# Kernel optimization log

Measured on AMD Instinct MI355X. Metric: run time of the kernel, lower is better.

The kernel has to match this reference:

```python
import jax, jax.numpy as jnp
import numpy as np

B, L, H, NH, T, WIN = 4, 4096, 256, 8, 64, 16
D = H // NH
NEG_SLOPE = 5.0
MASK_FILL = -1e12


def _leaky(x):
    return jnp.where(x >= 0, x, NEG_SLOPE * x)


def _window_indices():
    # static numpy index construction, mirrors EdgeBlock.self_attn
    off_u = np.concatenate([np.zeros(WIN + 1, np.int64), np.arange(1, WIN + 1)])
    off_d = np.concatenate([np.arange(-WIN, 0), np.zeros(WIN + 1, np.int64)])
    idx_u = np.arange(L)[:, None] + off_u  # [L, 2W+1]
    idx_d = np.arange(L)[:, None] + off_d  # [L, 2W+1]
    idx_mask = (idx_d >= 0) & (idx_u < L)
    return idx_u % L, idx_d % L, idx_mask


def setup_inputs() -> dict:
    key = jax.random.key(0)
    ks = jax.random.split(key, 12)
    s = 1.0 / np.sqrt(H)
    lengths = jnp.array([L, L - 128, L - 512, L - 1024])
    context_mask = jnp.arange(L)[None, :] < lengths[:, None]  # [B, L] bool
    return {
        'context': jax.random.normal(ks[0], (B, L, H), jnp.float32),
        'types': jax.random.normal(ks[1], (B, T, H), jnp.float32),
        'context_mask': context_mask,
        'W_types': jax.random.normal(ks[2], (H, H), jnp.float32) * s,
        'b_types': jnp.zeros((H,), jnp.float32),
        'W_context': jax.random.normal(ks[3], (H, H), jnp.float32) * s,
        'b_context': jnp.zeros((H,), jnp.float32),
        'upon': jax.random.normal(ks[4], (NH, D), jnp.float32) * s,
        'down': jax.random.normal(ks[5], (NH, D), jnp.float32) * s,
        'cross': jax.random.normal(ks[6], (NH, D, D), jnp.float32) * s,
        'W_out': jax.random.normal(ks[7], (H, H), jnp.float32) * s,
        'b_out': jnp.zeros((H,), jnp.float32),
    }


def reference(context, types, context_mask, W_types, b_types, W_context, b_context,
              upon, down, cross, W_out, b_out):
    idx_u, idx_d, idx_mask = _window_indices()

    # head-split projections
    types_h = (types @ W_types + b_types).reshape(B, T, NH, D)      # [B,T,n,d]
    context_h = (context @ W_context + b_context).reshape(B, L, NH, D)  # [B,L,n,d]

    # ---- cross attention scores: context queries over types (EdgeBlock.cross_attn)
    upon_q = jnp.einsum('blnd,nd->bnl', context_h, upon)
    down_t = jnp.einsum('btnd,nd->bnt', types_h, down)
    concat_ct = upon_q[..., None] + down_t[:, :, None, :]           # [B,n,L,T]
    prod_ct = jnp.einsum('blnd,ndh,btnh->bnlt', context_h, cross, types_h)
    types_s = _leaky(concat_ct + prod_ct)                            # [B,n,L,T]

    # ---- windowed self attention scores (EdgeBlock.self_attn)
    down_s = jnp.einsum('blnd,nd->bnl', context_h, down)
    concat_self = upon_q[:, :, idx_u] + down_s[:, :, idx_d]          # [B,n,L,2W+1]
    win_idx = idx_u  # source: cat([indices_d[:, :0], indices_u[:, 0:]]) == indices_u
    wmask = context_mask[:, win_idx] & idx_mask                      # [B,L,2W+1]
    value_h = context_h[:, win_idx]                                  # [B,L,2W+1,n,d]
    prod_self = jnp.einsum('blnd,ndh,blvnh->bnlv', context_h, cross, value_h)
    context_s = jnp.where(wmask[:, None], _leaky(concat_self + prod_self), MASK_FILL)

    # ---- joint softmax over types + window, then aggregate
    weights = jax.nn.softmax(jnp.concatenate([types_s, context_s], axis=-1), axis=-1)
    types_w, context_w = weights[..., :T], weights[..., T:]
    upd_t = jnp.einsum('bnlt,btnd->blnd', types_w, types_h)
    upd_c = jnp.einsum('bnlv,blvnd->blnd', context_w, value_h)
    update = (upd_t + upd_c).reshape(B, L, H)

    # residual + output transform (no_gate=True path: Linear + Tanh)
    return jnp.tanh((update + context) @ W_out + b_out)
```

## Files before the change

### kernel.cpp

```cpp
#include <hip/hip_runtime.h>
#include <cstdint>

#define Bq 4
#define Lq 4096
#define Hq 256
#define NHq 8
#define Tq 64
#define WINq 16
#define Dq 32
#define NSLOTS 33
#define NEG_SLOPE 5.0f
#define MASK_FILL -1e12f
#define TLq 64
#define MB 16

typedef __attribute__((ext_vector_type(8))) short short8;
typedef __attribute__((ext_vector_type(4))) float f32x4;

__device__ __forceinline__ float leaky(float x) { return x >= 0.f ? x : NEG_SLOPE * x; }

__device__ __forceinline__ uint16_t f2bf(float x) {
    uint32_t u = __float_as_uint(x);
    uint32_t r = (u + 0x7fffu + ((u >> 16) & 1u)) >> 16;
    return (uint16_t)r;
}
__device__ __forceinline__ float bf2f(uint16_t h) {
    return __uint_as_float(((uint32_t)h) << 16);
}

__global__ void k_prep(const float* __restrict__ Wc, const float* __restrict__ Wo,
                       uint16_t* __restrict__ pc_hi, uint16_t* __restrict__ pc_lo,
                       uint16_t* __restrict__ po_hi, uint16_t* __restrict__ po_lo,
                       const float* __restrict__ types, const float* __restrict__ Wt,
                       const float* __restrict__ bt, const float* __restrict__ down,
                       float* __restrict__ types_h, float* __restrict__ types_hT,
                       float* __restrict__ down_t) {
    __shared__ float sin[Hq];
    __shared__ float outr[Hq];
    if (blockIdx.x < 128) {
        int wsel = blockIdx.x >> 6;
        int blk = blockIdx.x & 63;
        const float* W = wsel ? Wo : Wc;
        uint16_t* ph = wsel ? po_hi : pc_hi;
        uint16_t* pl = wsel ? po_lo : pc_lo;
        int base = blk * 1024;
        for (int idx = base + threadIdx.x; idx < base + 1024; idx += 256) {
            int j = idx & 7, l = (idx >> 3) & 63, fragi = idx >> 9;
            int kc = fragi & 7, nt = fragi >> 3;
            int k = kc * 32 + (l >> 4) * 8 + j;
            int c = nt * 16 + (l & 15);
            float x = W[k * Hq + c];
            uint16_t h = f2bf(x);
            ph[idx] = h;
            pl[idx] = f2bf(x - bf2f(h));
        }
        return;
    }
    int row = blockIdx.x - 128;
    int h = threadIdx.x;
    int b = row >> 6, t = row & 63;
    sin[h] = types[(size_t)row * Hq + h];
    __syncthreads();
    float acc = bt[h];
    for (int k = 0; k < Hq; k += 4) {
        float4 iv = *(const float4*)&sin[k];
        acc = fmaf(iv.x, Wt[(k + 0) * Hq + h], acc);
        acc = fmaf(iv.y, Wt[(k + 1) * Hq + h], acc);
        acc = fmaf(iv.z, Wt[(k + 2) * Hq + h], acc);
        acc = fmaf(iv.w, Wt[(k + 3) * Hq + h], acc);
    }
    types_h[(size_t)row * Hq + h] = acc;
    types_hT[(size_t)(b * Hq + h) * Tq + t] = acc;
    outr[h] = acc;
    __syncthreads();
    if (h < NHq) {
        float s = 0.f;
        for (int d = 0; d < Dq; ++d) s += outr[h * Dq + d] * down[h * Dq + d];
        down_t[(b * NHq + h) * Tq + t] = s;
    }
}

#define APAD 264
#define OPAD 258
__global__ void __launch_bounds__(256) k_ctx(
        const float* __restrict__ ctx,
        const uint16_t* __restrict__ wp_hi, const uint16_t* __restrict__ wp_lo,
        const float* __restrict__ bc, const float* __restrict__ upon,
        const float* __restrict__ down,
        float* __restrict__ ctx_hT, float* __restrict__ uq,
        float* __restrict__ dsv) {
    int row0 = blockIdx.x * MB;
    int b = row0 >> 12, l0 = row0 & (Lq - 1);
    int tid = threadIdx.x;
    int w = tid >> 6, l = tid & 63;
    __shared__ __align__(16) char smem_raw[MB * APAD * 4];
    uint16_t* a_hi = (uint16_t*)smem_raw;
    uint16_t* a_lo = a_hi + MB * APAD;
    float* outb = (float*)smem_raw;

    {
        const float4* src = (const float4*)(ctx + (size_t)row0 * Hq);
#pragma unroll
        for (int j = 0; j < 4; ++j) {
            int f = tid + j * 256;
            int r = f >> 6, cg = f & 63;
            float4 v = src[f];
            uint16_t h0 = f2bf(v.x), h1 = f2bf(v.y), h2 = f2bf(v.z), h3 = f2bf(v.w);
            ushort4 hh = {h0, h1, h2, h3};
            ushort4 ll = {f2bf(v.x - bf2f(h0)), f2bf(v.y - bf2f(h1)),
                          f2bf(v.z - bf2f(h2)), f2bf(v.w - bf2f(h3))};
            *(ushort4*)&a_hi[r * APAD + cg * 4] = hh;
            *(ushort4*)&a_lo[r * APAD + cg * 4] = ll;
        }
    }
    __syncthreads();

    int nt0 = w * 4;
    int m = l & 15, quad = l >> 4;
    f32x4 acc[4];
#pragma unroll
    for (int t = 0; t < 4; ++t) acc[t] = (f32x4){0.f, 0.f, 0.f, 0.f};
#pragma unroll
    for (int kc = 0; kc < 8; ++kc) {
        short8 ah = *(const short8*)&a_hi[m * APAD + kc * 32 + quad * 8];
        short8 al = *(const short8*)&a_lo[m * APAD + kc * 32 + quad * 8];
#pragma unroll
        for (int t = 0; t < 4; ++t) {
            int fragi = (nt0 + t) * 8 + kc;
            short8 wh = *(const short8*)&wp_hi[fragi * 512 + l * 8];
            short8 wl = *(const short8*)&wp_lo[fragi * 512 + l * 8];
            acc[t] = __builtin_amdgcn_mfma_f32_16x16x32_bf16(ah, wh, acc[t], 0, 0, 0);
            acc[t] = __builtin_amdgcn_mfma_f32_16x16x32_bf16(ah, wl, acc[t], 0, 0, 0);
            acc[t] = __builtin_amdgcn_mfma_f32_16x16x32_bf16(al, wh, acc[t], 0, 0, 0);
        }
    }
    __syncthreads();

#pragma unroll
    for (int t = 0; t < 4; ++t) {
        int col = (nt0 + t) * 16 + m;
        float bv = bc[col];
#pragma unroll
        for (int r = 0; r < 4; ++r)
            outb[(quad * 4 + r) * OPAD + col] = acc[t][r] + bv;
    }
    __syncthreads();

    if (tid < MB * NHq) {
        int r = tid >> 3, n = tid & 7;
        float su = 0.f, sd = 0.f;
        for (int d = 0; d < Dq; ++d) {
            float v = outb[r * OPAD + n * Dq + d];
            su += v * upon[n * Dq + d];
            sd += v * down[n * Dq + d];
        }
        uq[(b * NHq + n) * Lq + l0 + r] = su;
        dsv[(b * NHq + n) * Lq + l0 + r] = sd;
    }
    {
        float* dst = ctx_hT + (size_t)(b * Hq + tid) * Lq + l0;
#pragma unroll
        for (int j = 0; j < MB / 4; ++j) {
            float4 o;
            o.x = outb[(4 * j + 0) * OPAD + tid];
            o.y = outb[(4 * j + 1) * OPAD + tid];
            o.z = outb[(4 * j + 2) * OPAD + tid];
            o.w = outb[(4 * j + 3) * OPAD + tid];
            ((float4*)dst)[j] = o;
        }
    }
}

__global__ void __launch_bounds__(256, 5) k_attn(
        const float* __restrict__ ctx_hT, const float* __restrict__ types_h,
        const float* __restrict__ types_hT, const float* __restrict__ cross,
        const float* __restrict__ uq, const float* __restrict__ dsv,
        const float* __restrict__ dt, const unsigned char* __restrict__ maskp,
        float* __restrict__ update) {
    int blk = blockIdx.x;
    int lt = blk & 63, n = (blk >> 6) & 7, b = blk >> 9;
    int l0 = lt * TLq;
    int tid = threadIdx.x;
    int ls = tid >> 2;
    int q  = tid & 3;
    int pl = l0 + ls;
    bool mask_b8 = (maskp[1] != 0);

    __shared__ float chx_s[32 * 97];
    __shared__ float crs_s[32 * 36];
    __shared__ float dots_s[64 * 19];
    __shared__ float tts2_s[64 * 36 + 16];
    __shared__ float uqe[96], dsve[96], maskf[96], dts[64];

    {
        int d = tid >> 3, k = tid & 7;
        const float* grow = ctx_hT + ((size_t)(b * NHq + n) * Dq + d) * Lq;
        float* lrow = &chx_s[d * 97 + k * 12];
        if (l0 >= 16 && l0 <= Lq - 80) {
            const float4* g = (const float4*)(grow + (l0 - 16) + k * 12);
            float4 v0 = g[0], v1 = g[1], v2 = g[2];
            lrow[0] = v0.x; lrow[1] = v0.y; lrow[2]  = v0.z; lrow[3]  = v0.w;
            lrow[4] = v1.x; lrow[5] = v1.y; lrow[6]  = v1.z; lrow[7]  = v1.w;
            lrow[8] = v2.x; lrow[9] = v2.y; lrow[10] = v2.z; lrow[11] = v2.w;
        } else {
#pragma unroll
            for (int m = 0; m < 12; ++m) {
                int gl = l0 - 16 + k * 12 + m;
                int glw = (gl < 0) ? gl + Lq : ((gl >= Lq) ? gl - Lq : gl);
                lrow[m] = grow[glw];
            }
        }
    }
    {
        float4 v = ((const float4*)(cross + n * (Dq * Dq)))[tid];
        float* p = &crs_s[(tid >> 3) * 36 + (tid & 7) * 4];
        p[0] = v.x; p[1] = v.y; p[2] = v.z; p[3] = v.w;
    }
    {
        int t = tid >> 2, c4 = tid & 3;
        const float4* src = (const float4*)(types_h + (size_t)(b * Tq + t) * Hq
                                            + n * Dq + 8 * c4);
        float* p = &tts2_s[t * 36 + 4 * (t >> 4) + 8 * c4];
        ((float4*)p)[0] = src[0];
        ((float4*)p)[1] = src[1];
    }
    if (tid < 96) {
        int gl = l0 - 16 + tid;
        int glw = (gl < 0) ? gl + Lq : ((gl >= Lq) ? gl - Lq : gl);
        uqe[tid] = uq[(b * NHq + n) * Lq + glw];
        unsigned char mb = mask_b8 ? maskp[b * Lq + glw]
                                   : maskp[(size_t)(b * Lq + glw) * 4];
        maskf[tid] = mb ? 1.f : 0.f;
    } else if (tid < 192) {
        int j = tid - 96;
        int gl = l0 - 16 + j;
        int glw = (gl < 0) ? gl + Lq : ((gl >= Lq) ? gl - Lq : gl);
        dsve[j] = dsv[(b * NHq + n) * Lq + glw];
    } else {
        dts[tid - 192] = dt[(b * NHq + n) * Tq + (tid - 192)];
    }
    __syncthreads();

    float a[8];
#pragma unroll
    for (int ii = 0; ii < 8; ++ii) a[ii] = 0.f;
#pragma unroll 2
    for (int d = 0; d < Dq; ++d) {
        float chv = chx_s[d * 97 + ls + 16];
        const float4* cp = (const float4*)(&crs_s[d * 36 + 8 * q]);
        float4 c0 = cp[0], c1 = cp[1];
        a[0] = fmaf(chv, c0.x, a[0]); a[1] = fmaf(chv, c0.y, a[1]);
        a[2] = fmaf(chv, c0.z, a[2]); a[3] = fmaf(chv, c0.w, a[3]);
        a[4] = fmaf(chv, c1.x, a[4]); a[5] = fmaf(chv, c1.y, a[5]);
        a[6] = fmaf(chv, c1.z, a[6]); a[7] = fmaf(chv, c1.w, a[7]);
    }

    float dot_self;
    {
#pragma unroll
        for (int u = 0; u < 17; ++u) {
            float acc = 0.f;
#pragma unroll
            for (int k = 0; k < 8; ++k)
                acc = fmaf(a[k], chx_s[(8 * q + k) * 97 + ls + 16 + u], acc);
            acc += __shfl_xor(acc, 1);
            acc += __shfl_xor(acc, 2);
            if (u == 0) dot_self = acc;
            else if (q == 0) dots_s[ls * 19 + u] = acc;
        }
    }

    float uq_l = uqe[ls + 16];
    float dsv_l = dsve[ls + 16];
    float cmask = maskf[ls + 16];

    int tb = 16 * q;
    float st[16];
#pragma unroll
    for (int j = 0; j < 16; ++j) st[j] = 0.f;
#pragma unroll
    for (int half = 0; half < 2; ++half) {
        float crf[16];
#pragma unroll
        for (int k = 0; k < 16; ++k)
            crf[k] = __shfl(a[k & 7], 2 * half + (k >> 3), 4);
#pragma unroll 4
        for (int j = 0; j < 16; ++j) {
            const float4* rp =
                (const float4*)&tts2_s[(tb + j) * 36 + 4 * q + 16 * half];
            float4 v0 = rp[0], v1 = rp[1], v2 = rp[2], v3 = rp[3];
            st[j] = fmaf(crf[0],  v0.x, st[j]); st[j] = fmaf(crf[1],  v0.y, st[j]);
            st[j] = fmaf(crf[2],  v0.z, st[j]); st[j] = fmaf(crf[3],  v0.w, st[j]);
            st[j] = fmaf(crf[4],  v1.x, st[j]); st[j] = fmaf(crf[5],  v1.y, st[j]);
            st[j] = fmaf(crf[6],  v1.z, st[j]); st[j] = fmaf(crf[7],  v1.w, st[j]);
            st[j] = fmaf(crf[8],  v2.x, st[j]); st[j] = fmaf(crf[9],  v2.y, st[j]);
            st[j] = fmaf(crf[10], v2.z, st[j]); st[j] = fmaf(crf[11], v2.w, st[j]);
            st[j] = fmaf(crf[12], v3.x, st[j]); st[j] = fmaf(crf[13], v3.y, st[j]);
            st[j] = fmaf(crf[14], v3.z, st[j]); st[j] = fmaf(crf[15], v3.w, st[j]);
        }
    }
#pragma unroll
    for (int j = 0; j < 16; ++j)
        st[j] = leaky(uq_l + dts[tb + j] + st[j]);

    int nv = (q == 0) ? 5 : 4;
    float su[4];
#pragma unroll
    for (int j = 0; j < 4; ++j) {
        int u = q + 1 + 4 * j;
        bool ok = (pl + u < Lq) && (maskf[ls + 16 + u] > 0.5f);
        su[j] = ok ? leaky(uqe[ls + 16 + u] + dsv_l + dots_s[ls * 19 + u])
                   : MASK_FILL;
    }

    float m = st[0];
#pragma unroll
    for (int j = 1; j < 16; ++j) m = fmaxf(m, st[j]);
#pragma unroll
    for (int j = 0; j < 5; ++j) {
        if (j < nv) {
            int v = q + 4 * j;
            if ((pl + v >= 16) && (cmask > 0.5f))
                m = fmaxf(m, leaky(uq_l + dsve[ls + v] + dot_self));
        }
    }
#pragma unroll
    for (int j = 0; j < 4; ++j) m = fmaxf(m, su[j]);
    m = fmaxf(m, __shfl_xor(m, 1));
    m = fmaxf(m, __shfl_xor(m, 2));
    float sum = 0.f, wself = 0.f;
#pragma unroll
    for (int j = 0; j < 16; ++j) { st[j] = __expf(st[j] - m); sum += st[j]; }
#pragma unroll
    for (int j = 0; j < 5; ++j) {
        if (j < nv) {
            int v = q + 4 * j;
            if ((pl + v >= 16) && (cmask > 0.5f)) {
                float e = __expf(leaky(uq_l + dsve[ls + v] + dot_self) - m);
                wself += e; sum += e;
            }
        }
    }
#pragma unroll
    for (int j = 0; j < 4; ++j)  { su[j] = __expf(su[j] - m); sum += su[j]; }
    sum += __shfl_xor(sum, 1);
    sum += __shfl_xor(sum, 2);
    float inv = 1.f / sum;
#pragma unroll
    for (int j = 0; j < 16; ++j) st[j] *= inv;
    wself *= inv;
#pragma unroll
    for (int j = 0; j < 4; ++j)  su[j] *= inv;

    float* dstrow = update + (size_t)(b * Lq + pl) * Hq + n * Dq;
#pragma unroll
    for (int c = 0; c < 4; ++c) {
        float u8[8];
#pragma unroll
        for (int e = 0; e < 8; ++e) u8[e] = 0.f;
#pragma unroll 2
        for (int j = 0; j < 16; ++j) {
            const float* vp = &tts2_s[(tb + j) * 36 + 4 * q + 8 * c];
            float4 a0 = ((const float4*)vp)[0];
            float4 a1 = ((const float4*)vp)[1];
            float wt = st[j];
            u8[0] = fmaf(wt, a0.x, u8[0]); u8[1] = fmaf(wt, a0.y, u8[1]);
            u8[2] = fmaf(wt, a0.z, u8[2]); u8[3] = fmaf(wt, a0.w, u8[3]);
            u8[4] = fmaf(wt, a1.x, u8[4]); u8[5] = fmaf(wt, a1.y, u8[5]);
            u8[6] = fmaf(wt, a1.z, u8[6]); u8[7] = fmaf(wt, a1.w, u8[7]);
        }
#pragma unroll
        for (int e = 0; e < 8; ++e)
            u8[e] = fmaf(wself, chx_s[(8 * c + e) * 97 + ls + 16], u8[e]);
#pragma unroll
        for (int j = 0; j < 4; ++j) {
            float wu = su[j];
            int u = q + 1 + 4 * j;
#pragma unroll
            for (int e = 0; e < 8; ++e)
                u8[e] = fmaf(wu, chx_s[(8 * c + e) * 97 + ls + 16 + u], u8[e]);
        }
#pragma unroll
        for (int e = 0; e < 8; ++e) {
            u8[e] += __shfl_xor(u8[e], 1);
            u8[e] += __shfl_xor(u8[e], 2);
        }
        if (q == c) {
            ((float4*)(dstrow + 8 * c))[0] = make_float4(u8[0], u8[1], u8[2], u8[3]);
            ((float4*)(dstrow + 8 * c))[1] = make_float4(u8[4], u8[5], u8[6], u8[7]);
        }
    }
}

__global__ void __launch_bounds__(256) k_out(
        const float* __restrict__ update, const float* __restrict__ ctx,
        const uint16_t* __restrict__ wp_hi, const uint16_t* __restrict__ wp_lo,
        const float* __restrict__ bo, float* __restrict__ out) {
    int row0 = blockIdx.x * MB;
    int tid = threadIdx.x;
    int w = tid >> 6, l = tid & 63;
    __shared__ __align__(16) char smem_raw[MB * APAD * 4];
    uint16_t* a_hi = (uint16_t*)smem_raw;
    uint16_t* a_lo = a_hi + MB * APAD;

    {
        const float4* s0 = (const float4*)(update + (size_t)row0 * Hq);
        const float4* s1 = (const float4*)(ctx + (size_t)row0 * Hq);
#pragma unroll
        for (int j = 0; j < 4; ++j) {
            int f = tid + j * 256;
            int r = f >> 6, cg = f & 63;
            float4 a = s0[f], bv = s1[f];
            float4 v; v.x = a.x + bv.x; v.y = a.y + bv.y;
            v.z = a.z + bv.z; v.w = a.w + bv.w;
            uint16_t h0 = f2bf(v.x), h1 = f2bf(v.y), h2 = f2bf(v.z), h3 = f2bf(v.w);
            ushort4 hh = {h0, h1, h2, h3};
            ushort4 ll = {f2bf(v.x - bf2f(h0)), f2bf(v.y - bf2f(h1)),
                          f2bf(v.z - bf2f(h2)), f2bf(v.w - bf2f(h3))};
            *(ushort4*)&a_hi[r * APAD + cg * 4] = hh;
            *(ushort4*)&a_lo[r * APAD + cg * 4] = ll;
        }
    }
    __syncthreads();

    int nt0 = w * 4;
    int m = l & 15, quad = l >> 4;
    f32x4 acc[4];
#pragma unroll
    for (int t = 0; t < 4; ++t) acc[t] = (f32x4){0.f, 0.f, 0.f, 0.f};
#pragma unroll
    for (int kc = 0; kc < 8; ++kc) {
        short8 ah = *(const short8*)&a_hi[m * APAD + kc * 32 + quad * 8];
        short8 al = *(const short8*)&a_lo[m * APAD + kc * 32 + quad * 8];
#pragma unroll
        for (int t = 0; t < 4; ++t) {
            int fragi = (nt0 + t) * 8 + kc;
            short8 wh = *(const short8*)&wp_hi[fragi * 512 + l * 8];
            short8 wl = *(const short8*)&wp_lo[fragi * 512 + l * 8];
            acc[t] = __builtin_amdgcn_mfma_f32_16x16x32_bf16(ah, wh, acc[t], 0, 0, 0);
            acc[t] = __builtin_amdgcn_mfma_f32_16x16x32_bf16(ah, wl, acc[t], 0, 0, 0);
            acc[t] = __builtin_amdgcn_mfma_f32_16x16x32_bf16(al, wh, acc[t], 0, 0, 0);
        }
    }
#pragma unroll
    for (int t = 0; t < 4; ++t) {
        int col = (nt0 + t) * 16 + m;
        float bv = bo[col];
#pragma unroll
        for (int r = 0; r < 4; ++r)
            out[(size_t)(row0 + quad * 4 + r) * Hq + col] = tanhf(acc[t][r] + bv);
    }
}

extern "C" void kernel_launch(void* const* d_in, const int* in_sizes, int n_in,
                              void* d_out, int out_size, void* d_ws, size_t ws_size,
                              hipStream_t stream) {
    const float* context   = (const float*)d_in[0];
    const float* types     = (const float*)d_in[1];
    const unsigned char* cmask = (const unsigned char*)d_in[2];
    const float* W_types   = (const float*)d_in[3];
    const float* b_types   = (const float*)d_in[4];
    const float* W_context = (const float*)d_in[5];
    const float* b_context = (const float*)d_in[6];
    const float* upon      = (const float*)d_in[7];
    const float* down      = (const float*)d_in[8];
    const float* cross     = (const float*)d_in[9];
    const float* W_out     = (const float*)d_in[10];
    const float* b_out     = (const float*)d_in[11];
    float* out = (float*)d_out;
    float* ws  = (float*)d_ws;

    float* ctx_hT   = ws;
    float* update   = ws + 4194304;
// ... 22 lines not shown
```

Baseline: 190.0 us.

## Compute attention aggregation with split-bf16 MFMA instead of scalar FMAs

Rewrites the weighted aggregation in k_attn (types weights times types values, window weights times context values) as 16x16x32 bf16 MFMA products. Each operand is split into hi and lo bf16 parts and three products are summed to keep near-fp32 accuracy. The window-score dot products stay in registers instead of a shared buffer. Shared memory is now one aliased buffer, which adds several barriers, and launch bounds drop from 5 to 4 blocks per SM. The added bf16 conversion cost and extra syncs may offset the reduced FMA and LDS traffic.

```diff
diff --git a/kernel.cpp b/kernel.cpp
--- a/kernel.cpp
+++ b/kernel.cpp
@@ -8,7 +8,6 @@
 #define Tq 64
 #define WINq 16
 #define Dq 32
-#define NSLOTS 33
 #define NEG_SLOPE 5.0f
 #define MASK_FILL -1e12f
 #define TLq 64
@@ -171,7 +170,11 @@
     }
 }
 
-__global__ void __launch_bounds__(256, 5) k_attn(
+#define WAT_STRIDE 72
+#define TTVT_STRIDE 72
+#define CHVT_STRIDE 104
+#define WAW_STRIDE 48
+__global__ void __launch_bounds__(256, 4) k_attn(
         const float* __restrict__ ctx_hT, const float* __restrict__ types_h,
         const float* __restrict__ types_hT, const float* __restrict__ cross,
         const float* __restrict__ uq, const float* __restrict__ dsv,
@@ -186,12 +189,24 @@
     int pl = l0 + ls;
     bool mask_b8 = (maskp[1] != 0);
 
-    __shared__ float chx_s[32 * 97];
-    __shared__ float crs_s[32 * 36];
-    __shared__ float dots_s[64 * 19];
-    __shared__ float tts2_s[64 * 36 + 16];
-    __shared__ float uqe[96], dsve[96], maskf[96], dts[64];
-
+    __shared__ __align__(16) char smem[36928];
+    float* chx_s  = (float*)(smem);
+    float* crs_s  = (float*)(smem + 12416);
+    float* tts2_s = (float*)(smem + 17024);
+    uint16_t* waT_hi  = (uint16_t*)(smem);
+    uint16_t* waT_lo  = (uint16_t*)(smem + 9216);
+    uint16_t* chvt_hi = (uint16_t*)(smem);
+    uint16_t* chvt_lo = (uint16_t*)(smem + 6656);
+    uint16_t* waw_hi  = (uint16_t*)(smem + 13312);
+    uint16_t* waw_lo  = (uint16_t*)(smem + 19456);
+    uint16_t* ttvt_hi = (uint16_t*)(smem + 26304);
+    uint16_t* ttvt_lo = (uint16_t*)(smem + 30912);
+    float* uqe   = (float*)(smem + 35520);
+    float* dsve  = (float*)(smem + 35904);
+    float* maskf = (float*)(smem + 36288);
+    float* dts   = (float*)(smem + 36672);
+
+    float chvv[12];
     {
         int d = tid >> 3, k = tid & 7;
         const float* grow = ctx_hT + ((size_t)(b * NHq + n) * Dq + d) * Lq;
@@ -199,17 +214,19 @@
         if (l0 >= 16 && l0 <= Lq - 80) {
             const float4* g = (const float4*)(grow + (l0 - 16) + k * 12);
             float4 v0 = g[0], v1 = g[1], v2 = g[2];
-            lrow[0] = v0.x; lrow[1] = v0.y; lrow[2]  = v0.z; lrow[3]  = v0.w;
-            lrow[4] = v1.x; lrow[5] = v1.y; lrow[6]  = v1.z; lrow[7]  = v1.w;
-            lrow[8] = v2.x; lrow[9] = v2.y; lrow[10] = v2.z; lrow[11] = v2.w;
+            chvv[0] = v0.x; chvv[1] = v0.y; chvv[2]  = v0.z; chvv[3]  = v0.w;
+            chvv[4] = v1.x; chvv[5] = v1.y; chvv[6]  = v1.z; chvv[7]  = v1.w;
+            chvv[8] = v2.x; chvv[9] = v2.y; chvv[10] = v2.z; chvv[11] = v2.w;
         } else {
 #pragma unroll
             for (int m = 0; m < 12; ++m) {
                 int gl = l0 - 16 + k * 12 + m;
                 int glw = (gl < 0) ? gl + Lq : ((gl >= Lq) ? gl - Lq : gl);
-                lrow[m] = grow[glw];
+                chvv[m] = grow[glw];
             }
         }
+#pragma unroll
+        for (int m = 0; m < 12; ++m) lrow[m] = chvv[m];
     }
     {
         float4 v = ((const float4*)(cross + n * (Dq * Dq)))[tid];
@@ -223,6 +240,23 @@
         float* p = &tts2_s[t * 36 + 4 * (t >> 4) + 8 * c4];
         ((float4*)p)[0] = src[0];
         ((float4*)p)[1] = src[1];
+    }
+    {
+        int d = tid >> 3, tc8 = (tid & 7) * 8;
+        const float* src = types_hT + ((size_t)(b * Hq) + n * Dq + d) * Tq + tc8;
+        float4 v0 = *(const float4*)src;
+        float4 v1 = *(const float4*)(src + 4);
+        float vv[8] = {v0.x, v0.y, v0.z, v0.w, v1.x, v1.y, v1.z, v1.w};
+        uint hp[4], lp[4];
+#pragma unroll
+        for (int jj = 0; jj < 4; ++jj) {
+            uint16_t h0 = f2bf(vv[2*jj]), h1 = f2bf(vv[2*jj+1]);
+            uint16_t e0 = f2bf(vv[2*jj] - bf2f(h0)), e1 = f2bf(vv[2*jj+1] - bf2f(h1));
+            hp[jj] = (uint)h0 | ((uint)h1 << 16);
+            lp[jj] = (uint)e0 | ((uint)e1 << 16);
+        }
+        *(uint4*)&ttvt_hi[d * TTVT_STRIDE + tc8] = make_uint4(hp[0], hp[1], hp[2], hp[3]);
+        *(uint4*)&ttvt_lo[d * TTVT_STRIDE + tc8] = make_uint4(lp[0], lp[1], lp[2], lp[3]);
     }
     if (tid < 96) {
         int gl = l0 - 16 + tid;
@@ -255,7 +289,7 @@
         a[6] = fmaf(chv, c1.z, a[6]); a[7] = fmaf(chv, c1.w, a[7]);
     }
 
-    float dot_self;
+    float dot_self, sud[4];
     {
 #pragma unroll
         for (int u = 0; u < 17; ++u) {
@@ -266,7 +300,7 @@
             acc += __shfl_xor(acc, 1);
             acc += __shfl_xor(acc, 2);
             if (u == 0) dot_self = acc;
-            else if (q == 0) dots_s[ls * 19 + u] = acc;
+            else if (((u - 1) & 3) == q) sud[(u - 1) >> 2] = acc;
         }
     }
 
@@ -309,7 +343,7 @@
     for (int j = 0; j < 4; ++j) {
         int u = q + 1 + 4 * j;
         bool ok = (pl + u < Lq) && (maskf[ls + 16 + u] > 0.5f);
-        su[j] = ok ? leaky(uqe[ls + 16 + u] + dsv_l + dots_s[ls * 19 + u])
+        su[j] = ok ? leaky(uqe[ls + 16 + u] + dsv_l + sud[j])
                    : MASK_FILL;
     }
 
@@ -351,44 +385,116 @@
     wself *= inv;
 #pragma unroll
     for (int j = 0; j < 4; ++j)  su[j] *= inv;
-
-    float* dstrow = update + (size_t)(b * Lq + pl) * Hq + n * Dq;
-#pragma unroll
-    for (int c = 0; c < 4; ++c) {
-        float u8[8];
-#pragma unroll
-        for (int e = 0; e < 8; ++e) u8[e] = 0.f;
-#pragma unroll 2
-        for (int j = 0; j < 16; ++j) {
-            const float* vp = &tts2_s[(tb + j) * 36 + 4 * q + 8 * c];
-            float4 a0 = ((const float4*)vp)[0];
-            float4 a1 = ((const float4*)vp)[1];
-            float wt = st[j];
-            u8[0] = fmaf(wt, a0.x, u8[0]); u8[1] = fmaf(wt, a0.y, u8[1]);
-            u8[2] = fmaf(wt, a0.z, u8[2]); u8[3] = fmaf(wt, a0.w, u8[3]);
-            u8[4] = fmaf(wt, a1.x, u8[4]); u8[5] = fmaf(wt, a1.y, u8[5]);
-            u8[6] = fmaf(wt, a1.z, u8[6]); u8[7] = fmaf(wt, a1.w, u8[7]);
-        }
-#pragma unroll
-        for (int e = 0; e < 8; ++e)
-            u8[e] = fmaf(wself, chx_s[(8 * c + e) * 97 + ls + 16], u8[e]);
+    wself += __shfl_xor(wself, 1);
+    wself += __shfl_xor(wself, 2);
+
+    __syncthreads();
+
+    {
+        uint hp[8], lp[8];
+#pragma unroll
+        for (int jj = 0; jj < 8; ++jj) {
+            uint16_t h0 = f2bf(st[2*jj]), h1 = f2bf(st[2*jj+1]);
+            uint16_t e0 = f2bf(st[2*jj] - bf2f(h0)), e1 = f2bf(st[2*jj+1] - bf2f(h1));
+            hp[jj] = (uint)h0 | ((uint)h1 << 16);
+            lp[jj] = (uint)e0 | ((uint)e1 << 16);
+        }
+        uint16_t* hb = &waT_hi[ls * WAT_STRIDE + tb];
+        uint16_t* lb = &waT_lo[ls * WAT_STRIDE + tb];
+        *(uint4*)hb       = make_uint4(hp[0], hp[1], hp[2], hp[3]);
+        *(uint4*)(hb + 8) = make_uint4(hp[4], hp[5], hp[6], hp[7]);
+        *(uint4*)lb       = make_uint4(lp[0], lp[1], lp[2], lp[3]);
+        *(uint4*)(lb + 8) = make_uint4(lp[4], lp[5], lp[6], lp[7]);
+    }
+    __syncthreads();
+
+    int wv = tid >> 6;
+    int lane = tid & 63;
+    int mrow = lane & 15, chunk = lane >> 4;
+    f32x4 acc0 = (f32x4){0.f, 0.f, 0.f, 0.f};
+    f32x4 acc1 = (f32x4){0.f, 0.f, 0.f, 0.f};
+#pragma unroll
+    for (int ks = 0; ks < 2; ++ks) {
+        short8 bh = *(const short8*)&waT_hi[(16*wv + mrow) * WAT_STRIDE + 32*ks + 8*chunk];
+        short8 bl = *(const short8*)&waT_lo[(16*wv + mrow) * WAT_STRIDE + 32*ks + 8*chunk];
+        short8 a0h = *(const short8*)&ttvt_hi[mrow * TTVT_STRIDE + 32*ks + 8*chunk];
+        short8 a0l = *(const short8*)&ttvt_lo[mrow * TTVT_STRIDE + 32*ks + 8*chunk];
+        short8 a1h = *(const short8*)&ttvt_hi[(16 + mrow) * TTVT_STRIDE + 32*ks + 8*chunk];
+        short8 a1l = *(const short8*)&ttvt_lo[(16 + mrow) * TTVT_STRIDE + 32*ks + 8*chunk];
+        acc0 = __builtin_amdgcn_mfma_f32_16x16x32_bf16(a0h, bh, acc0, 0, 0, 0);
+        acc0 = __builtin_amdgcn_mfma_f32_16x16x32_bf16(a0l, bh, acc0, 0, 0, 0);
+        acc0 = __builtin_amdgcn_mfma_f32_16x16x32_bf16(a0h, bl, acc0, 0, 0, 0);
+        acc1 = __builtin_amdgcn_mfma_f32_16x16x32_bf16(a1h, bh, acc1, 0, 0, 0);
+        acc1 = __builtin_amdgcn_mfma_f32_16x16x32_bf16(a1l, bh, acc1, 0, 0, 0);
+        acc1 = __builtin_amdgcn_mfma_f32_16x16x32_bf16(a1h, bl, acc1, 0, 0, 0);
+    }
+    __syncthreads();
+
+    {
+        int d = tid >> 3, k = tid & 7;
+        uint hp[6], lp[6];
+#pragma unroll
+        for (int jj = 0; jj < 6; ++jj) {
+            uint16_t h0 = f2bf(chvv[2*jj]), h1 = f2bf(chvv[2*jj+1]);
+            uint16_t e0 = f2bf(chvv[2*jj] - bf2f(h0)), e1 = f2bf(chvv[2*jj+1] - bf2f(h1));
+            hp[jj] = (uint)h0 | ((uint)h1 << 16);
+            lp[jj] = (uint)e0 | ((uint)e1 << 16);
+        }
+        uint16_t* hb = &chvt_hi[d * CHVT_STRIDE + k * 12];
+        uint16_t* lb = &chvt_lo[d * CHVT_STRIDE + k * 12];
+        *(uint2*)(hb)     = make_uint2(hp[0], hp[1]);
+        *(uint2*)(hb + 4) = make_uint2(hp[2], hp[3]);
+        *(uint2*)(hb + 8) = make_uint2(hp[4], hp[5]);
+        *(uint2*)(lb)     = make_uint2(lp[0], lp[1]);
+        *(uint2*)(lb + 4) = make_uint2(lp[2], lp[3]);
+        *(uint2*)(lb + 8) = make_uint2(lp[4], lp[5]);
+    }
+    {
+        float4 z = make_float4(0.f, 0.f, 0.f, 0.f);
+        float4* wz = (float4*)waw_hi;
+        for (int i = tid; i < 768; i += 256) wz[i] = z;
+    }
+    __syncthreads();
+
+    {
+        int jself = (ls & 15) + 16;
 #pragma unroll
         for (int j = 0; j < 4; ++j) {
-            float wu = su[j];
-            int u = q + 1 + 4 * j;
-#pragma unroll
-            for (int e = 0; e < 8; ++e)
-                u8[e] = fmaf(wu, chx_s[(8 * c + e) * 97 + ls + 16 + u], u8[e]);
-        }
-#pragma unroll
-        for (int e = 0; e < 8; ++e) {
-            u8[e] += __shfl_xor(u8[e], 1);
-            u8[e] += __shfl_xor(u8[e], 2);
-        }
-        if (q == c) {
-            ((float4*)(dstrow + 8 * c))[0] = make_float4(u8[0], u8[1], u8[2], u8[3]);
-            ((float4*)(dstrow + 8 * c))[1] = make_float4(u8[4], u8[5], u8[6], u8[7]);
-        }
+            int col = jself + q + 1 + 4 * j;
+            float v = su[j];
+            uint16_t h = f2bf(v);
+            waw_hi[ls * WAW_STRIDE + col] = h;
+            waw_lo[ls * WAW_STRIDE + col] = f2bf(v - bf2f(h));
+        }
+        if (q == 0) {
+            uint16_t h = f2bf(wself);
+            waw_hi[ls * WAW_STRIDE + jself] = h;
+            waw_lo[ls * WAW_STRIDE + jself] = f2bf(wself - bf2f(h));
+        }
+    }
+    __syncthreads();
+
+    {
+        short8 bh = *(const short8*)&waw_hi[(16*wv + mrow) * WAW_STRIDE + 16 + 8*chunk];
+        short8 bl = *(const short8*)&waw_lo[(16*wv + mrow) * WAW_STRIDE + 16 + 8*chunk];
+        int kabs = 16*wv + 16 + 8*chunk;
+        short8 a0h = *(const short8*)&chvt_hi[mrow * CHVT_STRIDE + kabs];
+        short8 a0l = *(const short8*)&chvt_lo[mrow * CHVT_STRIDE + kabs];
+        short8 a1h = *(const short8*)&chvt_hi[(16 + mrow) * CHVT_STRIDE + kabs];
+        short8 a1l = *(const short8*)&chvt_lo[(16 + mrow) * CHVT_STRIDE + kabs];
+        acc0 = __builtin_amdgcn_mfma_f32_16x16x32_bf16(a0h, bh, acc0, 0, 0, 0);
+        acc0 = __builtin_amdgcn_mfma_f32_16x16x32_bf16(a0l, bh, acc0, 0, 0, 0);
+        acc0 = __builtin_amdgcn_mfma_f32_16x16x32_bf16(a0h, bl, acc0, 0, 0, 0);
+        acc1 = __builtin_amdgcn_mfma_f32_16x16x32_bf16(a1h, bh, acc1, 0, 0, 0);
+        acc1 = __builtin_amdgcn_mfma_f32_16x16x32_bf16(a1l, bh, acc1, 0, 0, 0);
+        acc1 = __builtin_amdgcn_mfma_f32_16x16x32_bf16(a1h, bl, acc1, 0, 0, 0);
+    }
+
+    {
+        int lcol = l0 + 16 * wv + mrow;
+        float* dst = update + (size_t)(b * Lq + lcol) * Hq + n * Dq + 4 * chunk;
+        *(float4*)dst        = make_float4(acc0[0], acc0[1], acc0[2], acc0[3]);
+        *(float4*)(dst + 16) = make_float4(acc1[0], acc1[1], acc1[2], acc1[3]);
     }
 }
 
```

Result: faster. 177.9 us (-6.4%).

## Rewrite attention kernel with split-bf16 MFMA matmuls for scores and aggregation

Applied to the files above, without the earlier changes.

Replaces the scalar FMA attention kernel with MFMA 16x16x32 bf16 instructions. Each fp32 operand is split into hi/lo bf16 pairs and combined with three MFMAs to keep close to fp32 accuracy. The cross projection, type scores, window scores and weighted aggregation all become small matrix products staged through a reused shared-memory buffer. The occupancy hint drops from 5 to 3 blocks per SU because of the larger shared footprint. The split-precision conversion and extra syncs add overhead and a small accuracy risk.

```diff
diff --git a/kernel.cpp b/kernel.cpp
--- a/kernel.cpp
+++ b/kernel.cpp
@@ -8,7 +8,6 @@
 #define Tq 64
 #define WINq 16
 #define Dq 32
-#define NSLOTS 33
 #define NEG_SLOPE 5.0f
 #define MASK_FILL -1e12f
 #define TLq 64
@@ -171,7 +170,7 @@
     }
 }
 
-__global__ void __launch_bounds__(256, 5) k_attn(
+__global__ void __launch_bounds__(256, 3) k_attn(
         const float* __restrict__ ctx_hT, const float* __restrict__ types_h,
         const float* __restrict__ types_hT, const float* __restrict__ cross,
         const float* __restrict__ uq, const float* __restrict__ dsv,
@@ -181,214 +180,327 @@
     int lt = blk & 63, n = (blk >> 6) & 7, b = blk >> 9;
     int l0 = lt * TLq;
     int tid = threadIdx.x;
-    int ls = tid >> 2;
-    int q  = tid & 3;
-    int pl = l0 + ls;
+    int g = tid >> 6;
+    int lane = tid & 63;
+    int Q = lane >> 4, s = lane & 15;
     bool mask_b8 = (maskp[1] != 0);
 
-    __shared__ float chx_s[32 * 97];
-    __shared__ float crs_s[32 * 36];
-    __shared__ float dots_s[64 * 19];
-    __shared__ float tts2_s[64 * 36 + 16];
-    __shared__ float uqe[96], dsve[96], maskf[96], dts[64];
-
-    {
-        int d = tid >> 3, k = tid & 7;
-        const float* grow = ctx_hT + ((size_t)(b * NHq + n) * Dq + d) * Lq;
-        float* lrow = &chx_s[d * 97 + k * 12];
-        if (l0 >= 16 && l0 <= Lq - 80) {
-            const float4* g = (const float4*)(grow + (l0 - 16) + k * 12);
-            float4 v0 = g[0], v1 = g[1], v2 = g[2];
-            lrow[0] = v0.x; lrow[1] = v0.y; lrow[2]  = v0.z; lrow[3]  = v0.w;
-            lrow[4] = v1.x; lrow[5] = v1.y; lrow[6]  = v1.z; lrow[7]  = v1.w;
-            lrow[8] = v2.x; lrow[9] = v2.y; lrow[10] = v2.z; lrow[11] = v2.w;
+    __shared__ __align__(16) char smem[53952];
+    uint16_t* TT_hi     = (uint16_t*)(smem);
+    uint16_t* TT_lo     = (uint16_t*)(smem + 5120);
+    uint16_t* chxT_hi   = (uint16_t*)(smem + 10240);
+    uint16_t* chxT_lo   = (uint16_t*)(smem + 16640);
+    uint16_t* waT_hi    = (uint16_t*)(smem);
+    uint16_t* waT_lo    = (uint16_t*)(smem + 9216);
+    uint16_t* crossT_hi = (uint16_t*)(smem + 23040);
+    uint16_t* crossT_lo = (uint16_t*)(smem + 25600);
+    uint16_t* crle_hi   = (uint16_t*)(smem + 23040);
+    uint16_t* crle_lo   = (uint16_t*)(smem + 28160);
+    uint16_t* waw_hi    = (uint16_t*)(smem + 23040);
+    uint16_t* waw_lo    = (uint16_t*)(smem + 28160);
+    uint16_t* chvt_hi   = (uint16_t*)(smem + 33280);
+    uint16_t* chvt_lo   = (uint16_t*)(smem + 38400);
+    uint16_t* ttvt_hi   = (uint16_t*)(smem + 43520);
+    uint16_t* ttvt_lo   = (uint16_t*)(smem + 48128);
+    float* uqe   = (float*)(smem + 52736);
+    float* dsve  = (float*)(smem + 53056);
+    float* maskf = (float*)(smem + 53376);
+    float* dts   = (float*)(smem + 53696);
+
+    {
+        int d_ = tid >> 3, k_ = tid & 7, base = k_ * 10;
+        const float* grow = ctx_hT + ((size_t)(b * NHq + n) * Dq + d_) * Lq;
+        float cv[10];
+        if (l0 <= Lq - 80) {
+            const float2* g2 = (const float2*)(grow + l0 + base);
+#pragma unroll
+            for (int j = 0; j < 5; ++j) { float2 v = g2[j]; cv[2*j] = v.x; cv[2*j+1] = v.y; }
         } else {
 #pragma unroll
-            for (int m = 0; m < 12; ++m) {
-                int gl = l0 - 16 + k * 12 + m;
-                int glw = (gl < 0) ? gl + Lq : ((gl >= Lq) ? gl - Lq : gl);
-                lrow[m] = grow[glw];
+            for (int m = 0; m < 10; ++m) {
+                int gl = l0 + base + m;
+                cv[m] = grow[gl >= Lq ? gl - Lq : gl];
             }
         }
-    }
-    {
+        uint16_t hh[10], ll[10];
+#pragma unroll
+        for (int m = 0; m < 10; ++m) {
+            hh[m] = f2bf(cv[m]);
+            ll[m] = f2bf(cv[m] - bf2f(hh[m]));
+        }
+#pragma unroll
+        for (int j = 0; j < 5; ++j) {
+            *(uint*)&chvt_hi[d_ * 80 + base + 2*j] = (uint)hh[2*j] | ((uint)hh[2*j+1] << 16);
+            *(uint*)&chvt_lo[d_ * 80 + base + 2*j] = (uint)ll[2*j] | ((uint)ll[2*j+1] << 16);
+        }
+#pragma unroll
+        for (int m = 0; m < 10; ++m) {
+            chxT_hi[(base + m) * 40 + d_] = hh[m];
+            chxT_lo[(base + m) * 40 + d_] = ll[m];
+        }
+    }
+    {
+        int d_ = tid >> 3, e4 = (tid & 7) * 4;
         float4 v = ((const float4*)(cross + n * (Dq * Dq)))[tid];
-        float* p = &crs_s[(tid >> 3) * 36 + (tid & 7) * 4];
-        p[0] = v.x; p[1] = v.y; p[2] = v.z; p[3] = v.w;
-    }
-    {
-        int t = tid >> 2, c4 = tid & 3;
-        const float4* src = (const float4*)(types_h + (size_t)(b * Tq + t) * Hq
-                                            + n * Dq + 8 * c4);
-        float* p = &tts2_s[t * 36 + 4 * (t >> 4) + 8 * c4];
-        ((float4*)p)[0] = src[0];
-        ((float4*)p)[1] = src[1];
-    }
-    if (tid < 96) {
-        int gl = l0 - 16 + tid;
-        int glw = (gl < 0) ? gl + Lq : ((gl >= Lq) ? gl - Lq : gl);
+        float vv[4] = {v.x, v.y, v.z, v.w};
+#pragma unroll
+        for (int j = 0; j < 4; ++j) {
+            uint16_t h = f2bf(vv[j]);
+            crossT_hi[(e4 + j) * 40 + d_] = h;
+            crossT_lo[(e4 + j) * 40 + d_] = f2bf(vv[j] - bf2f(h));
+        }
+    }
+    {
+        int t = tid >> 2, c8 = (tid & 3) * 8;
+        const float* src = types_h + (size_t)(b * Tq + t) * Hq + n * Dq + c8;
+        float4 v0 = *(const float4*)src, v1 = *(const float4*)(src + 4);
+        float vv[8] = {v0.x, v0.y, v0.z, v0.w, v1.x, v1.y, v1.z, v1.w};
+        uint hp[4], lp[4];
+#pragma unroll
+        for (int j = 0; j < 4; ++j) {
+            uint16_t h0 = f2bf(vv[2*j]), h1 = f2bf(vv[2*j+1]);
+            hp[j] = (uint)h0 | ((uint)h1 << 16);
+            lp[j] = (uint)f2bf(vv[2*j] - bf2f(h0)) | ((uint)f2bf(vv[2*j+1] - bf2f(h1)) << 16);
+        }
+        *(uint4*)&TT_hi[t * 40 + c8] = make_uint4(hp[0], hp[1], hp[2], hp[3]);
+        *(uint4*)&TT_lo[t * 40 + c8] = make_uint4(lp[0], lp[1], lp[2], lp[3]);
+    }
+    {
+        int d_ = tid >> 3, t8 = (tid & 7) * 8;
+        const float* src = types_hT + ((size_t)(b * Hq) + n * Dq + d_) * Tq + t8;
+        float4 v0 = *(const float4*)src, v1 = *(const float4*)(src + 4);
+        float vv[8] = {v0.x, v0.y, v0.z, v0.w, v1.x, v1.y, v1.z, v1.w};
+        uint hp[4], lp[4];
+#pragma unroll
+        for (int j = 0; j < 4; ++j) {
+            uint16_t h0 = f2bf(vv[2*j]), h1 = f2bf(vv[2*j+1]);
+            hp[j] = (uint)h0 | ((uint)h1 << 16);
+            lp[j] = (uint)f2bf(vv[2*j] - bf2f(h0)) | ((uint)f2bf(vv[2*j+1] - bf2f(h1)) << 16);
+        }
+        *(uint4*)&ttvt_hi[d_ * 72 + t8] = make_uint4(hp[0], hp[1], hp[2], hp[3]);
+        *(uint4*)&ttvt_lo[d_ * 72 + t8] = make_uint4(lp[0], lp[1], lp[2], lp[3]);
+    }
+    if (tid < 80) {
+        int gl = l0 + tid;
+        int glw = gl >= Lq ? gl - Lq : gl;
         uqe[tid] = uq[(b * NHq + n) * Lq + glw];
         unsigned char mb = mask_b8 ? maskp[b * Lq + glw]
                                    : maskp[(size_t)(b * Lq + glw) * 4];
         maskf[tid] = mb ? 1.f : 0.f;
-    } else if (tid < 192) {
-        int j = tid - 96;
-        int gl = l0 - 16 + j;
-        int glw = (gl < 0) ? gl + Lq : ((gl >= Lq) ? gl - Lq : gl);
-        dsve[j] = dsv[(b * NHq + n) * Lq + glw];
-    } else {
+    } else if (tid >= 96 && tid < 176) {
+        int i = tid - 96;
+        int gl = l0 - 16 + i;
+        int glw = gl < 0 ? gl + Lq : (gl >= Lq ? gl - Lq : gl);
+        dsve[i] = dsv[(b * NHq + n) * Lq + glw];
+    } else if (tid >= 192) {
         dts[tid - 192] = dt[(b * NHq + n) * Tq + (tid - 192)];
     }
     __syncthreads();
 
-    float a[8];
-#pragma unroll
-    for (int ii = 0; ii < 8; ++ii) a[ii] = 0.f;
-#pragma unroll 2
-    for (int d = 0; d < Dq; ++d) {
-        float chv = chx_s[d * 97 + ls + 16];
-        const float4* cp = (const float4*)(&crs_s[d * 36 + 8 * q]);
-        float4 c0 = cp[0], c1 = cp[1];
-        a[0] = fmaf(chv, c0.x, a[0]); a[1] = fmaf(chv, c0.y, a[1]);
-        a[2] = fmaf(chv, c0.z, a[2]); a[3] = fmaf(chv, c0.w, a[3]);
-        a[4] = fmaf(chv, c1.x, a[4]); a[5] = fmaf(chv, c1.y, a[5]);
-        a[6] = fmaf(chv, c1.z, a[6]); a[7] = fmaf(chv, c1.w, a[7]);
-    }
-
-    float dot_self;
-    {
-#pragma unroll
-        for (int u = 0; u < 17; ++u) {
-            float acc = 0.f;
-#pragma unroll
-            for (int k = 0; k < 8; ++k)
-                acc = fmaf(a[k], chx_s[(8 * q + k) * 97 + ls + 16 + u], acc);
-            acc += __shfl_xor(acc, 1);
-            acc += __shfl_xor(acc, 2);
-            if (u == 0) dot_self = acc;
-            else if (q == 0) dots_s[ls * 19 + u] = acc;
-        }
-    }
-
-    float uq_l = uqe[ls + 16];
-    float dsv_l = dsve[ls + 16];
-    float cmask = maskf[ls + 16];
-
-    int tb = 16 * q;
-    float st[16];
-#pragma unroll
-    for (int j = 0; j < 16; ++j) st[j] = 0.f;
-#pragma unroll
-    for (int half = 0; half < 2; ++half) {
-        float crf[16];
-#pragma unroll
-        for (int k = 0; k < 16; ++k)
-            crf[k] = __shfl(a[k & 7], 2 * half + (k >> 3), 4);
-#pragma unroll 4
-        for (int j = 0; j < 16; ++j) {
-            const float4* rp =
-                (const float4*)&tts2_s[(tb + j) * 36 + 4 * q + 16 * half];
-            float4 v0 = rp[0], v1 = rp[1], v2 = rp[2], v3 = rp[3];
-            st[j] = fmaf(crf[0],  v0.x, st[j]); st[j] = fmaf(crf[1],  v0.y, st[j]);
-            st[j] = fmaf(crf[2],  v0.z, st[j]); st[j] = fmaf(crf[3],  v0.w, st[j]);
-            st[j] = fmaf(crf[4],  v1.x, st[j]); st[j] = fmaf(crf[5],  v1.y, st[j]);
-            st[j] = fmaf(crf[6],  v1.z, st[j]); st[j] = fmaf(crf[7],  v1.w, st[j]);
-            st[j] = fmaf(crf[8],  v2.x, st[j]); st[j] = fmaf(crf[9],  v2.y, st[j]);
-            st[j] = fmaf(crf[10], v2.z, st[j]); st[j] = fmaf(crf[11], v2.w, st[j]);
-            st[j] = fmaf(crf[12], v3.x, st[j]); st[j] = fmaf(crf[13], v3.y, st[j]);
-            st[j] = fmaf(crf[14], v3.z, st[j]); st[j] = fmaf(crf[15], v3.w, st[j]);
-        }
-    }
-#pragma unroll
-    for (int j = 0; j < 16; ++j)
-        st[j] = leaky(uq_l + dts[tb + j] + st[j]);
-
-    int nv = (q == 0) ? 5 : 4;
-    float su[4];
-#pragma unroll
-    for (int j = 0; j < 4; ++j) {
-        int u = q + 1 + 4 * j;
-        bool ok = (pl + u < Lq) && (maskf[ls + 16 + u] > 0.5f);
-        su[j] = ok ? leaky(uqe[ls + 16 + u] + dsv_l + dots_s[ls * 19 + u])
-                   : MASK_FILL;
-    }
-
-    float m = st[0];
-#pragma unroll
-    for (int j = 1; j < 16; ++j) m = fmaxf(m, st[j]);
-#pragma unroll
-    for (int j = 0; j < 5; ++j) {
-        if (j < nv) {
-            int v = q + 4 * j;
-            if ((pl + v >= 16) && (cmask > 0.5f))
-                m = fmaxf(m, leaky(uq_l + dsve[ls + v] + dot_self));
-        }
-    }
-#pragma unroll
-    for (int j = 0; j < 4; ++j) m = fmaxf(m, su[j]);
-    m = fmaxf(m, __shfl_xor(m, 1));
-    m = fmaxf(m, __shfl_xor(m, 2));
-    float sum = 0.f, wself = 0.f;
-#pragma unroll
-    for (int j = 0; j < 16; ++j) { st[j] = __expf(st[j] - m); sum += st[j]; }
-#pragma unroll
-    for (int j = 0; j < 5; ++j) {
-        if (j < nv) {
-            int v = q + 4 * j;
-            if ((pl + v >= 16) && (cmask > 0.5f)) {
-                float e = __expf(leaky(uq_l + dsve[ls + v] + dot_self) - m);
-                wself += e; sum += e;
-            }
-        }
-    }
-#pragma unroll
-    for (int j = 0; j < 4; ++j)  { su[j] = __expf(su[j] - m); sum += su[j]; }
-    sum += __shfl_xor(sum, 1);
-    sum += __shfl_xor(sum, 2);
-    float inv = 1.f / sum;
-#pragma unroll
-    for (int j = 0; j < 16; ++j) st[j] *= inv;
-    wself *= inv;
-#pragma unroll
-    for (int j = 0; j < 4; ++j)  su[j] *= inv;
-
-    float* dstrow = update + (size_t)(b * Lq + pl) * Hq + n * Dq;
-#pragma unroll
-    for (int c = 0; c < 4; ++c) {
-        float u8[8];
-#pragma unroll
-        for (int e = 0; e < 8; ++e) u8[e] = 0.f;
-#pragma unroll 2
-        for (int j = 0; j < 16; ++j) {
-            const float* vp = &tts2_s[(tb + j) * 36 + 4 * q + 8 * c];
-            float4 a0 = ((const float4*)vp)[0];
-            float4 a1 = ((const float4*)vp)[1];
-            float wt = st[j];
-            u8[0] = fmaf(wt, a0.x, u8[0]); u8[1] = fmaf(wt, a0.y, u8[1]);
-            u8[2] = fmaf(wt, a0.z, u8[2]); u8[3] = fmaf(wt, a0.w, u8[3]);
-            u8[4] = fmaf(wt, a1.x, u8[4]); u8[5] = fmaf(wt, a1.y, u8[5]);
-            u8[6] = fmaf(wt, a1.z, u8[6]); u8[7] = fmaf(wt, a1.w, u8[7]);
-        }
-#pragma unroll
-        for (int e = 0; e < 8; ++e)
-            u8[e] = fmaf(wself, chx_s[(8 * c + e) * 97 + ls + 16], u8[e]);
-#pragma unroll
-        for (int j = 0; j < 4; ++j) {
-            float wu = su[j];
-            int u = q + 1 + 4 * j;
-#pragma unroll
-            for (int e = 0; e < 8; ++e)
-                u8[e] = fmaf(wu, chx_s[(8 * c + e) * 97 + ls + 16 + u], u8[e]);
-        }
-#pragma unroll
-        for (int e = 0; e < 8; ++e) {
-            u8[e] += __shfl_xor(u8[e], 1);
-            u8[e] += __shfl_xor(u8[e], 2);
-        }
-        if (q == c) {
-            ((float4*)(dstrow + 8 * c))[0] = make_float4(u8[0], u8[1], u8[2], u8[3]);
-            ((float4*)(dstrow + 8 * c))[1] = make_float4(u8[4], u8[5], u8[6], u8[7]);
-        }
+    f32x4 cr0 = (f32x4){0.f, 0.f, 0.f, 0.f};
+    f32x4 cr1 = (f32x4){0.f, 0.f, 0.f, 0.f};
+    {
+        short8 axh = *(const short8*)&chxT_hi[(16*g + s) * 40 + 8*Q];
+        short8 axl = *(const short8*)&chxT_lo[(16*g + s) * 40 + 8*Q];
+        short8 b0h = *(const short8*)&crossT_hi[s * 40 + 8*Q];
+        short8 b0l = *(const short8*)&crossT_lo[s * 40 + 8*Q];
+        short8 b1h = *(const short8*)&crossT_hi[(16 + s) * 40 + 8*Q];
+        short8 b1l = *(const short8*)&crossT_lo[(16 + s) * 40 + 8*Q];
+        cr0 = __builtin_amdgcn_mfma_f32_16x16x32_bf16(axh, b0h, cr0, 0, 0, 0);
+        cr0 = __builtin_amdgcn_mfma_f32_16x16x32_bf16(axl, b0h, cr0, 0, 0, 0);
+        cr0 = __builtin_amdgcn_mfma_f32_16x16x32_bf16(axh, b0l, cr0, 0, 0, 0);
+        cr1 = __builtin_amdgcn_mfma_f32_16x16x32_bf16(axh, b1h, cr1, 0, 0, 0);
+        cr1 = __builtin_amdgcn_mfma_f32_16x16x32_bf16(axl, b1h, cr1, 0, 0, 0);
+        cr1 = __builtin_amdgcn_mfma_f32_16x16x32_bf16(axh, b1l, cr1, 0, 0, 0);
+    }
+    __syncthreads();
+
+#pragma unroll
+    for (int r = 0; r < 4; ++r) {
+        int row = 16*g + 4*Q + r;
+        uint16_t h0 = f2bf(cr0[r]);
+        crle_hi[row * 40 + s] = h0;
+        crle_lo[row * 40 + s] = f2bf(cr0[r] - bf2f(h0));
+        uint16_t h1 = f2bf(cr1[r]);
+        crle_hi[row * 40 + 16 + s] = h1;
+        crle_lo[row * 40 + 16 + s] = f2bf(cr1[r] - bf2f(h1));
+    }
+
+    f32x4 p2[4], p3[2];
+#pragma unroll
+    for (int c = 0; c < 4; ++c) p2[c] = (f32x4){0.f, 0.f, 0.f, 0.f};
+#pragma unroll
+    for (int t_ = 0; t_ < 2; ++t_) p3[t_] = (f32x4){0.f, 0.f, 0.f, 0.f};
+    {
+        short8 cah = *(const short8*)&crle_hi[(16*g + s) * 40 + 8*Q];
+        short8 cal = *(const short8*)&crle_lo[(16*g + s) * 40 + 8*Q];
+#pragma unroll
+        for (int c = 0; c < 4; ++c) {
+            short8 bh = *(const short8*)&TT_hi[(s + 16*c) * 40 + 8*Q];
+            short8 bl = *(const short8*)&TT_lo[(s + 16*c) * 40 + 8*Q];
+            p2[c] = __builtin_amdgcn_mfma_f32_16x16x32_bf16(cah, bh, p2[c], 0, 0, 0);
+            p2[c] = __builtin_amdgcn_mfma_f32_16x16x32_bf16(cal, bh, p2[c], 0, 0, 0);
+            p2[c] = __builtin_amdgcn_mfma_f32_16x16x32_bf16(cah, bl, p2[c], 0, 0, 0);
+        }
+#pragma unroll
+        for (int t_ = 0; t_ < 2; ++t_) {
+            short8 bh = *(const short8*)&chxT_hi[(16*g + 16*t_ + s) * 40 + 8*Q];
+            short8 bl = *(const short8*)&chxT_lo[(16*g + 16*t_ + s) * 40 + 8*Q];
+            p3[t_] = __builtin_amdgcn_mfma_f32_16x16x32_bf16(cah, bh, p3[t_], 0, 0, 0);
+            p3[t_] = __builtin_amdgcn_mfma_f32_16x16x32_bf16(cal, bh, p3[t_], 0, 0, 0);
+            p3[t_] = __builtin_amdgcn_mfma_f32_16x16x32_bf16(cah, bl, p3[t_], 0, 0, 0);
+        }
+    }
+
+    float uqr[4], cmr[4], dsr[4], dd[4];
+    *(float4*)uqr = *(const float4*)&uqe[16*g + 4*Q];
+    *(float4*)cmr = *(const float4*)&maskf[16*g + 4*Q];
+    *(float4*)dsr = *(const float4*)&dsve[16*g + 4*Q + 16];
+#pragma unroll
+    for (int r = 0; r < 4; ++r) dd[r] = dsve[16*g + 4*Q + s + r];
+    float dtv[4], uw[2], mw[2];
+#pragma unroll
+    for (int c = 0; c < 4; ++c) dtv[c] = dts[s + 16*c];
+#pragma unroll
+    for (int t_ = 0; t_ < 2; ++t_) {
+        uw[t_] = uqe[16*g + s + 16*t_];
+        mw[t_] = maskf[16*g + s + 16*t_];
+    }
+    float dsb[4];
+#pragma unroll
+    for (int r = 0; r < 4; ++r) dsb[r] = __shfl(p3[0][r], 20*Q + r);
+
+    float stt[4][4], rup[2][4], rdn[4], rdn16[4];
+#pragma unroll
+    for (int c = 0; c < 4; ++c)
+#pragma unroll
+        for (int r = 0; r < 4; ++r)
+            stt[c][r] = leaky(uqr[r] + dtv[c] + p2[c][r]);
+#pragma unroll
+    for (int t_ = 0; t_ < 2; ++t_)
+#pragma unroll
+        for (int r = 0; r < 4; ++r) {
+            int u = s + 16*t_ - 4*Q - r;
+            bool ok = (u >= 1) && (u <= 16) && (l0 + 16*g + s + 16*t_ < Lq)
+                      && (mw[t_] > 0.5f);
+            rup[t_][r] = ok ? leaky(uw[t_] + dsr[r] + p3[t_][r]) : MASK_FILL;
+        }
+#pragma unroll
+    for (int r = 0; r < 4; ++r) {
+        bool okd = (l0 + 16*g + 4*Q + r + s >= 16) && (cmr[r] > 0.5f);
+        rdn[r]   = okd ? leaky(uqr[r] + dd[r] + dsb[r]) : MASK_FILL;
+        rdn16[r] = (s == 0 && cmr[r] > 0.5f) ? leaky(uqr[r] + dsr[r] + dsb[r])
+                                             : MASK_FILL;
+    }
+
+    float mx[4];
+#pragma unroll
+    for (int r = 0; r < 4; ++r) {
+        float m = fmaxf(fmaxf(stt[0][r], stt[1][r]), fmaxf(stt[2][r], stt[3][r]));
+        m = fmaxf(m, fmaxf(rup[0][r], rup[1][r]));
+        m = fmaxf(m, fmaxf(rdn[r], rdn16[r]));
+        mx[r] = m;
+    }
+#pragma unroll
+    for (int msk = 1; msk <= 8; msk <<= 1)
+#pragma unroll
+        for (int r = 0; r < 4; ++r) mx[r] = fmaxf(mx[r], __shfl_xor(mx[r], msk));
+
+    float sTU[4] = {0.f, 0.f, 0.f, 0.f}, sD[4];
+#pragma unroll
+    for (int c = 0; c < 4; ++c)
+#pragma unroll
+        for (int r = 0; r < 4; ++r) {
+            stt[c][r] = __expf(stt[c][r] - mx[r]);
+            sTU[r] += stt[c][r];
+        }
+#pragma unroll
+    for (int t_ = 0; t_ < 2; ++t_)
+#pragma unroll
+        for (int r = 0; r < 4; ++r) {
+            rup[t_][r] = __expf(rup[t_][r] - mx[r]);
+            sTU[r] += rup[t_][r];
+        }
+#pragma unroll
+    for (int r = 0; r < 4; ++r) {
+        rdn[r] = __expf(rdn[r] - mx[r]);
+        rdn16[r] = __expf(rdn16[r] - mx[r]);
+        sD[r] = rdn[r] + rdn16[r];
+    }
+#pragma unroll
+    for (int msk = 1; msk <= 8; msk <<= 1)
+#pragma unroll
+        for (int r = 0; r < 4; ++r) {
+            sTU[r] += __shfl_xor(sTU[r], msk);
+            sD[r]  += __shfl_xor(sD[r], msk);
+        }
+    float inv[4], wself[4];
+#pragma unroll
+    for (int r = 0; r < 4; ++r) {
+        inv[r] = 1.f / (sTU[r] + sD[r]);
+        wself[r] = sD[r] * inv[r];
+    }
+
+    __syncthreads();
+
+#pragma unroll
+    for (int r = 0; r < 4; ++r) {
+        int row = 16*g + 4*Q + r;
+#pragma unroll
+        for (int c = 0; c < 4; ++c) {
+            float v = stt[c][r] * inv[r];
+            uint16_t h = f2bf(v);
+            waT_hi[row * 72 + s + 16*c] = h;
+            waT_lo[row * 72 + s + 16*c] = f2bf(v - bf2f(h));
+        }
+#pragma unroll
+        for (int t_ = 0; t_ < 2; ++t_) {
+            int u = s + 16*t_ - 4*Q - r;
+            float v = (u == 0) ? wself[r]
+                    : ((u >= 1 && u <= 16) ? rup[t_][r] * inv[r] : 0.f);
+            uint16_t h = f2bf(v);
+            waw_hi[row * 40 + s + 16*t_] = h;
+            waw_lo[row * 40 + s + 16*t_] = f2bf(v - bf2f(h));
+        }
+    }
+
+    f32x4 a0 = (f32x4){0.f, 0.f, 0.f, 0.f};
+    f32x4 a1 = (f32x4){0.f, 0.f, 0.f, 0.f};
+#pragma unroll
+    for (int ks = 0; ks < 2; ++ks) {
+        short8 bh = *(const short8*)&waT_hi[(16*g + s) * 72 + 32*ks + 8*Q];
+        short8 bl = *(const short8*)&waT_lo[(16*g + s) * 72 + 32*ks + 8*Q];
+        short8 t0h = *(const short8*)&ttvt_hi[s * 72 + 32*ks + 8*Q];
+        short8 t0l = *(const short8*)&ttvt_lo[s * 72 + 32*ks + 8*Q];
+        short8 t1h = *(const short8*)&ttvt_hi[(16 + s) * 72 + 32*ks + 8*Q];
+        short8 t1l = *(const short8*)&ttvt_lo[(16 + s) * 72 + 32*ks + 8*Q];
+        a0 = __builtin_amdgcn_mfma_f32_16x16x32_bf16(t0h, bh, a0, 0, 0, 0);
+        a0 = __builtin_amdgcn_mfma_f32_16x16x32_bf16(t0l, bh, a0, 0, 0, 0);
+        a0 = __builtin_amdgcn_mfma_f32_16x16x32_bf16(t0h, bl, a0, 0, 0, 0);
+        a1 = __builtin_amdgcn_mfma_f32_16x16x32_bf16(t1h, bh, a1, 0, 0, 0);
+        a1 = __builtin_amdgcn_mfma_f32_16x16x32_bf16(t1l, bh, a1, 0, 0, 0);
+        a1 = __builtin_amdgcn_mfma_f32_16x16x32_bf16(t1h, bl, a1, 0, 0, 0);
+    }
+    {
+        short8 wbh = *(const short8*)&waw_hi[(16*g + s) * 40 + 8*Q];
+        short8 wbl = *(const short8*)&waw_lo[(16*g + s) * 40 + 8*Q];
+        short8 c0h = *(const short8*)&chvt_hi[s * 80 + 16*g + 8*Q];
+        short8 c0l = *(const short8*)&chvt_lo[s * 80 + 16*g + 8*Q];
+        short8 c1h = *(const short8*)&chvt_hi[(16 + s) * 80 + 16*g + 8*Q];
+        short8 c1l = *(const short8*)&chvt_lo[(16 + s) * 80 + 16*g + 8*Q];
+        a0 = __builtin_amdgcn_mfma_f32_16x16x32_bf16(c0h, wbh, a0, 0, 0, 0);
+        a0 = __builtin_amdgcn_mfma_f32_16x16x32_bf16(c0l, wbh, a0, 0, 0, 0);
+        a0 = __builtin_amdgcn_mfma_f32_16x16x32_bf16(c0h, wbl, a0, 0, 0, 0);
+        a1 = __builtin_amdgcn_mfma_f32_16x16x32_bf16(c1h, wbh, a1, 0, 0, 0);
+        a1 = __builtin_amdgcn_mfma_f32_16x16x32_bf16(c1l, wbh, a1, 0, 0, 0);
+        a1 = __builtin_amdgcn_mfma_f32_16x16x32_bf16(c1h, wbl, a1, 0, 0, 0);
+    }
+
+    {
+        int lcol = l0 + 16*g + s;
+        float* dst = update + (size_t)(b * Lq + lcol) * Hq + n * Dq + 4*Q;
+        *(float4*)dst        = make_float4(a0[0], a0[1], a0[2], a0[3]);
+        *(float4*)(dst + 16) = make_float4(a1[0], a1[1], a1[2], a1[3]);
     }
 }
 
```

After: 166.0 us. -12.7%, faster.
